# Kernel tuning notes

Measured on AMD Instinct MI355X. Metric: run time of the kernel, lower is better.

## Reference

```python
import jax, jax.numpy as jnp
import numpy as np

B, C = 16384, 1000

def setup_inputs() -> dict:
    key = jax.random.key(0)
    k1, k2, k3 = jax.random.split(key, 3)
    out = jax.random.normal(k1, (B, C), dtype=jnp.float32)
    target = jax.random.randint(k2, (B,), 0, C, dtype=jnp.int64)
    # noise transition matrix: positive entries (row-normalization not required by the math)
    T = jax.random.uniform(k3, (C, C), dtype=jnp.float32)
    return {"out": out, "target": target, "T": T}

def reference(out, target, T):
    # softmax probabilities and log-probs, each computed once for the whole batch
    p = jax.nn.softmax(out, axis=1)            # [B, C]
    logp = jax.nn.log_softmax(out, axis=1)     # [B, C]
    idx = jnp.arange(out.shape[0])
    pro1 = p[idx, target]                      # p_i[y_i]
    # torch: (T.t() @ p_i.t()).t()[:, y_i] == (p_i @ T)[y_i]
    pro2 = (p @ T)[idx, target]                # [B]
    # beta is wrapped in a fresh Variable in torch -> no grad flows through it
    beta = jax.lax.stop_gradient(pro1 / pro2)
    ce = -logp[idx, target]                    # per-sample cross entropy
    # reduction='sum' (default)
    return jnp.sum(beta * ce)
```

## Files before the change

kernel.cpp:

```cpp
#include <hip/hip_runtime.h>
#include <math.h>

#define C 1000
#define C4 250

typedef float v4f __attribute__((ext_vector_type(4)));

__device__ __forceinline__ float wave_reduce_sum(float v) {
#pragma unroll
  for (int off = 32; off > 0; off >>= 1) v += __shfl_xor(v, off, 64);
  return v;
}

__global__ __launch_bounds__(256) void transpose_k(
    const float* __restrict__ A, float* __restrict__ At) {
  __shared__ float tile[32][33];
  int x = blockIdx.x * 32 + threadIdx.x;
#pragma unroll
  for (int k = 0; k < 32; k += 8) {
    int y = blockIdx.y * 32 + threadIdx.y + k;
    if (x < C && y < C)
      tile[threadIdx.y + k][threadIdx.x] =
          __builtin_nontemporal_load(&A[(size_t)y * C + x]);
  }
  __syncthreads();
  int xt = blockIdx.y * 32 + threadIdx.x;
#pragma unroll
  for (int k = 0; k < 32; k += 8) {
    int yt = blockIdx.x * 32 + threadIdx.y + k;
    if (xt < C && yt < C) At[(size_t)yt * C + xt] = tile[threadIdx.x][threadIdx.y + k];
  }
}

__global__ __launch_bounds__(256) void reweight_k(
    const float* __restrict__ xin, const int* __restrict__ target,
    const float* __restrict__ Tt, float* __restrict__ partial, int B) {
  int wid = threadIdx.x >> 6;
  int lane = threadIdx.x & 63;
  int row = blockIdx.x * 4 + wid;
  float contrib = 0.0f;
  if (row < B) {
    int y = target[row];
    const v4f* x4 = (const v4f*)(xin + (size_t)row * C);
    const v4f* t4 = (const v4f*)(Tt + (size_t)y * C);
    v4f v[4], t[4];
#pragma unroll
    for (int k = 0; k < 4; k++) {
      int j = lane + k * 64;
      if (j < C4) {
        v[k] = __builtin_nontemporal_load(&x4[j]);
        t[k] = t4[j];
      }
    }
    float se = 0.0f, st = 0.0f;
#pragma unroll
    for (int k = 0; k < 4; k++) {
      int j = lane + k * 64;
      if (j < C4) {
        float e0 = __expf(v[k].x), e1 = __expf(v[k].y);
        float e2 = __expf(v[k].z), e3 = __expf(v[k].w);
        se += (e0 + e1) + (e2 + e3);
        st += e0 * t[k].x + e1 * t[k].y + e2 * t[k].z + e3 * t[k].w;
      }
    }
    int jy = y >> 2;
    int kk = jy >> 6, sl = jy & 63, cc = y & 3;
    v4f vk = v[0];
    if (kk == 1) vk = v[1];
    else if (kk == 2) vk = v[2];
    else if (kk == 3) vk = v[3];
    float xl = (cc == 0) ? vk.x : (cc == 1) ? vk.y : (cc == 2) ? vk.z : vk.w;
    float xy = __shfl(xl, sl, 64);
    se = wave_reduce_sum(se);
    st = wave_reduce_sum(st);
    if (lane == 0) contrib = (__expf(xy) / st) * (logf(se) - xy);
  }
  __shared__ float bsum[4];
  if (lane == 0) bsum[wid] = contrib;
  __syncthreads();
  if (threadIdx.x == 0)
    partial[blockIdx.x] = (bsum[0] + bsum[1]) + (bsum[2] + bsum[3]);
}

__global__ __launch_bounds__(256) void reduce_k(const float* __restrict__ partial,
                                                float* __restrict__ result, int n) {
  float s = 0.0f;
  for (int i = threadIdx.x; i < n; i += 256) s += partial[i];
  s = wave_reduce_sum(s);
  __shared__ float b[4];
  if ((threadIdx.x & 63) == 0) b[threadIdx.x >> 6] = s;
  __syncthreads();
  if (threadIdx.x == 0) *result = (b[0] + b[1]) + (b[2] + b[3]);
}

__global__ void zero_k(float* __restrict__ result) { *result = 0.0f; }

__global__ __launch_bounds__(256) void reweight_cols_k(
    const float* __restrict__ xin, const int* __restrict__ target,
    const float* __restrict__ Tmat, float* __restrict__ result, int B) {
  int wid = threadIdx.x >> 6, lane = threadIdx.x & 63;
  int row = blockIdx.x * 4 + wid;
  float contrib = 0.0f;
  if (row < B) {
    int y = target[row];
    const v4f* x4 = (const v4f*)(xin + (size_t)row * C);
    float se = 0.0f, st = 0.0f;
    float xy = 0.0f;
#pragma unroll
    for (int k = 0; k < 4; k++) {
      int j = lane + k * 64;
      if (j < C4) {
        v4f v = x4[j];
        int jb = j * 4;
        float e0 = __expf(v.x), e1 = __expf(v.y), e2 = __expf(v.z), e3 = __expf(v.w);
        se += (e0 + e1) + (e2 + e3);
        st += e0 * Tmat[(size_t)(jb + 0) * C + y] +
              e1 * Tmat[(size_t)(jb + 1) * C + y] +
              e2 * Tmat[(size_t)(jb + 2) * C + y] +
              e3 * Tmat[(size_t)(jb + 3) * C + y];
      }
    }
    se = wave_reduce_sum(se);
    st = wave_reduce_sum(st);
    if (lane == 0) {
      xy = xin[(size_t)row * C + y];
      contrib = (__expf(xy) / st) * (logf(se) - xy);
    }
  }
  __shared__ float bsum[4];
  if (lane == 0) bsum[wid] = contrib;
  __syncthreads();
  if (threadIdx.x == 0) {
    float s = (bsum[0] + bsum[1]) + (bsum[2] + bsum[3]);
    atomicAdd(result, s);
  }
}

extern "C" void kernel_launch(void* const* d_in, const int* in_sizes, int n_in,
                              void* d_out, int out_size, void* d_ws, size_t ws_size,
                              hipStream_t stream) {
  const float* xin = (const float*)d_in[0];
  const int* target = (const int*)d_in[1];
  const float* T = (const float*)d_in[2];
  float* result = (float*)d_out;
  int B = in_sizes[1];
  int nblocks = (B + 3) / 4;

  size_t tt_bytes = (size_t)C * C * sizeof(float);
  size_t need = tt_bytes + (size_t)nblocks * sizeof(float);

  if (ws_size >= need) {
    float* Tt = (float*)d_ws;
    float* partial = (float*)((char*)d_ws + tt_bytes);
    transpose_k<<<dim3(32, 32), dim3(32, 8), 0, stream>>>(T, Tt);
    reweight_k<<<nblocks, 256, 0, stream>>>(xin, target, Tt, partial, B);
    reduce_k<<<1, 256, 0, stream>>>(partial, result, nblocks);
  } else {
    zero_k<<<1, 1, 0, stream>>>(result);
    reweight_cols_k<<<nblocks, 256, 0, stream>>>(xin, target, T, result, B);
  }
}
```

Baseline: 112.7 us.

## Fuse transpose, reweight and reduction into one cooperative kernel with grid sync

Replaces the three-kernel sequence (transpose, per-row reweight, final reduce) with one cooperatively launched kernel of 1024 blocks. The blocks transpose T, synchronize across the grid, then grid-stride over rows and atomically add per-block sums into the result. This removes two kernel launches and the partial-sum buffer round trip. In exchange it adds grid-sync cost, caps parallelism at 1024 persistent blocks, and makes the float summation order nondeterministic through atomics.

```diff
diff --git a/kernel.cpp b/kernel.cpp
--- a/kernel.cpp
+++ b/kernel.cpp
@@ -1,5 +1,8 @@
 #include <hip/hip_runtime.h>
+#include <hip/hip_cooperative_groups.h>
 #include <math.h>
+
+namespace cg = cooperative_groups;
 
 #define C 1000
 #define C4 250
@@ -12,34 +15,40 @@
   return v;
 }
 
-__global__ __launch_bounds__(256) void transpose_k(
-    const float* __restrict__ A, float* __restrict__ At) {
-  __shared__ float tile[32][33];
-  int x = blockIdx.x * 32 + threadIdx.x;
+__global__ __launch_bounds__(256, 4) void fused_k(
+    const float* __restrict__ xin, const int* __restrict__ target,
+    const float* __restrict__ T, float* __restrict__ Tt,
+    float* __restrict__ result, int B) {
+  cg::grid_group grid = cg::this_grid();
+
+  {
+    __shared__ float tile[32][33];
+    int tx = threadIdx.x & 31, ty = threadIdx.x >> 5;
+    int bx = blockIdx.x & 31, by = blockIdx.x >> 5;
+    if (blockIdx.x == 0 && threadIdx.x == 0) *result = 0.0f;
+    int x = bx * 32 + tx;
 #pragma unroll
-  for (int k = 0; k < 32; k += 8) {
-    int y = blockIdx.y * 32 + threadIdx.y + k;
-    if (x < C && y < C)
-      tile[threadIdx.y + k][threadIdx.x] =
-          __builtin_nontemporal_load(&A[(size_t)y * C + x]);
+    for (int k = 0; k < 32; k += 8) {
+      int y = by * 32 + ty + k;
+      if (x < C && y < C)
+        tile[ty + k][tx] = __builtin_nontemporal_load(&T[(size_t)y * C + x]);
+    }
+    __syncthreads();
+    int xt = by * 32 + tx;
+#pragma unroll
+    for (int k = 0; k < 32; k += 8) {
+      int yt = bx * 32 + ty + k;
+      if (xt < C && yt < C) Tt[(size_t)yt * C + xt] = tile[tx][ty + k];
+    }
   }
-  __syncthreads();
-  int xt = blockIdx.y * 32 + threadIdx.x;
-#pragma unroll
-  for (int k = 0; k < 32; k += 8) {
-    int yt = blockIdx.x * 32 + threadIdx.y + k;
-    if (xt < C && yt < C) At[(size_t)yt * C + xt] = tile[threadIdx.x][threadIdx.y + k];
-  }
-}
+  grid.sync();
 
-__global__ __launch_bounds__(256) void reweight_k(
-    const float* __restrict__ xin, const int* __restrict__ target,
-    const float* __restrict__ Tt, float* __restrict__ partial, int B) {
   int wid = threadIdx.x >> 6;
   int lane = threadIdx.x & 63;
-  int row = blockIdx.x * 4 + wid;
-  float contrib = 0.0f;
-  if (row < B) {
+  int nwaves = gridDim.x * 4;
+  int wgid = blockIdx.x * 4 + wid;
+  float acc = 0.0f;
+  for (int row = wgid; row < B; row += nwaves) {
     int y = target[row];
     const v4f* x4 = (const v4f*)(xin + (size_t)row * C);
     const v4f* t4 = (const v4f*)(Tt + (size_t)y * C);
@@ -73,24 +82,13 @@
     float xy = __shfl(xl, sl, 64);
     se = wave_reduce_sum(se);
     st = wave_reduce_sum(st);
-    if (lane == 0) contrib = (__expf(xy) / st) * (logf(se) - xy);
+    if (lane == 0) acc += (__expf(xy) / st) * (logf(se) - xy);
   }
   __shared__ float bsum[4];
-  if (lane == 0) bsum[wid] = contrib;
+  if (lane == 0) bsum[wid] = acc;
   __syncthreads();
   if (threadIdx.x == 0)
-    partial[blockIdx.x] = (bsum[0] + bsum[1]) + (bsum[2] + bsum[3]);
-}
-
-__global__ __launch_bounds__(256) void reduce_k(const float* __restrict__ partial,
-                                                float* __restrict__ result, int n) {
-  float s = 0.0f;
-  for (int i = threadIdx.x; i < n; i += 256) s += partial[i];
-  s = wave_reduce_sum(s);
-  __shared__ float b[4];
-  if ((threadIdx.x & 63) == 0) b[threadIdx.x >> 6] = s;
-  __syncthreads();
-  if (threadIdx.x == 0) *result = (b[0] + b[1]) + (b[2] + b[3]);
+    atomicAdd(result, (bsum[0] + bsum[1]) + (bsum[2] + bsum[3]));
 }
 
 __global__ void zero_k(float* __restrict__ result) { *result = 0.0f; }
@@ -105,7 +103,6 @@
     int y = target[row];
     const v4f* x4 = (const v4f*)(xin + (size_t)row * C);
     float se = 0.0f, st = 0.0f;
-    float xy = 0.0f;
 #pragma unroll
     for (int k = 0; k < 4; k++) {
       int j = lane + k * 64;
@@ -123,17 +120,15 @@
     se = wave_reduce_sum(se);
     st = wave_reduce_sum(st);
     if (lane == 0) {
-      xy = xin[(size_t)row * C + y];
+      float xy = xin[(size_t)row * C + y];
       contrib = (__expf(xy) / st) * (logf(se) - xy);
     }
   }
   __shared__ float bsum[4];
   if (lane == 0) bsum[wid] = contrib;
   __syncthreads();
-  if (threadIdx.x == 0) {
-    float s = (bsum[0] + bsum[1]) + (bsum[2] + bsum[3]);
-    atomicAdd(result, s);
-  }
+  if (threadIdx.x == 0)
+    atomicAdd(result, (bsum[0] + bsum[1]) + (bsum[2] + bsum[3]));
 }
 
 extern "C" void kernel_launch(void* const* d_in, const int* in_sizes, int n_in,
@@ -144,18 +139,17 @@
   const float* T = (const float*)d_in[2];
   float* result = (float*)d_out;
   int B = in_sizes[1];
-  int nblocks = (B + 3) / 4;
 
   size_t tt_bytes = (size_t)C * C * sizeof(float);
-  size_t need = tt_bytes + (size_t)nblocks * sizeof(float);
 
-  if (ws_size >= need) {
+  if (ws_size >= tt_bytes) {
     float* Tt = (float*)d_ws;
-    float* partial = (float*)((char*)d_ws + tt_bytes);
-    transpose_k<<<dim3(32, 32), dim3(32, 8), 0, stream>>>(T, Tt);
-    reweight_k<<<nblocks, 256, 0, stream>>>(xin, target, Tt, partial, B);
-    reduce_k<<<1, 256, 0, stream>>>(partial, result, nblocks);
+    void* args[] = {(void*)&xin, (void*)&target, (void*)&T,
+                    (void*)&Tt, (void*)&result, (void*)&B};
+    hipLaunchCooperativeKernel((void*)fused_k, dim3(1024), dim3(256), args, 0,
+                               stream);
   } else {
+    int nblocks = (B + 3) / 4;
     zero_k<<<1, 1, 0, stream>>>(result);
     reweight_cols_k<<<nblocks, 256, 0, stream>>>(xin, target, T, result, B);
   }
```

After: 207.3 us. 84.0% more time.
